# Optimization experiments

Hardware: AMD Instinct MI355X
Metric: run time of the kernel (lower is better)

## Reference

```python
import jax, jax.numpy as jnp
from jax import lax
import numpy as np

H_FEAT = 14
W_FEAT = 14
BN_EPS = 1e-5
NORM_EPS = 1e-12

def _coord_tensor():
    # Python-2 integer division as in the original repo
    c = np.zeros((H_FEAT * W_FEAT, 2), dtype=np.float32)
    for i in range(H_FEAT * W_FEAT):
        c[i, 0] = (i // W_FEAT - H_FEAT // 2) / (H_FEAT / 2.0)
        c[i, 1] = (i % W_FEAT - W_FEAT // 2) / (W_FEAT / 2.0)
    return jnp.asarray(c.reshape(1, H_FEAT, W_FEAT, 2).transpose(0, 3, 1, 2))  # [1,2,14,14]

def _l2norm(x, axis):
    n = jnp.linalg.norm(x, axis=axis, keepdims=True)
    return x / jnp.maximum(n, NORM_EPS)

def _conv2d(x, w, b, pad):
    y = lax.conv_general_dilated(x, w, (1, 1), [(pad, pad), (pad, pad)],
                                 dimension_numbers=("NCHW", "OIHW", "NCHW"))
    return y + b[None, :, None, None]

def _bn_train(x, g, b):
    m = x.mean(axis=(0, 2, 3), keepdims=True)
    v = x.var(axis=(0, 2, 3), keepdims=True)
    return (x - m) * lax.rsqrt(v + BN_EPS) * g[None, :, None, None] + b[None, :, None, None]

def _lstm_scan(emb, Wih, Whh, bih, bhh):
    # emb: [T, B, 300]; PyTorch gate order i,f,g,o
    Hdim = Whh.shape[1]
    B = emb.shape[1]
    def step(carry, x):
        h, c = carry
        gates = x @ Wih.T + h @ Whh.T + bih + bhh  # [B, 4H]
        i, f, g, o = jnp.split(gates, 4, axis=-1)
        c = jax.nn.sigmoid(f) * c + jax.nn.sigmoid(i) * jnp.tanh(g)
        h = jax.nn.sigmoid(o) * jnp.tanh(c)
        return (h, c), h
    init = (jnp.zeros((B, Hdim), emb.dtype), jnp.zeros((B, Hdim), emb.dtype))
    _, hs = lax.scan(step, init, emb)
    return hs  # [T, B, H]

def _resblock(v, coord, c1w, c1b, c2w, c2b, bng, bnb):
    B = v.shape[0]
    vin = jnp.concatenate([v, jnp.broadcast_to(coord, (B, 2, H_FEAT, W_FEAT))], axis=1)
    v1 = jax.nn.relu(_conv2d(vin, c1w, c1b, 0))
    v2 = jax.nn.relu(_bn_train(_conv2d(v1, c2w, c2b, 1), bng, bnb))
    return v2 + v1

def setup_inputs() -> dict:
    key = jax.random.key(0)
    ks = jax.random.split(key, 24)
    B, T, V, E = 128, 45, 10000, 300
    Hh = 1024
    s = 0.02
    inp = {}
    inp["que"] = jax.random.randint(ks[0], (B, T), 0, V, dtype=jnp.int64)
    inp["img"] = jax.random.normal(ks[1], (B, 1024, H_FEAT, W_FEAT), dtype=jnp.float32)
    inp["lookup"] = s * jax.random.normal(ks[2], (V + 1, E), dtype=jnp.float32)
    inp["Wih_f"] = s * jax.random.normal(ks[3], (4 * Hh, E), dtype=jnp.float32)
    inp["Whh_f"] = s * jax.random.normal(ks[4], (4 * Hh, Hh), dtype=jnp.float32)
    inp["bih_f"] = jnp.zeros((4 * Hh,), jnp.float32)
    inp["bhh_f"] = jnp.zeros((4 * Hh,), jnp.float32)
    inp["Wih_b"] = s * jax.random.normal(ks[5], (4 * Hh, E), dtype=jnp.float32)
    inp["Whh_b"] = s * jax.random.normal(ks[6], (4 * Hh, Hh), dtype=jnp.float32)
    inp["bih_b"] = jnp.zeros((4 * Hh,), jnp.float32)
    inp["bhh_b"] = jnp.zeros((4 * Hh,), jnp.float32)
    inp["conv0_w"] = s * jax.random.normal(ks[7], (128, 1026, 3, 3), dtype=jnp.float32)
    inp["conv0_b"] = jnp.zeros((128,), jnp.float32)
    inp["bn0_g"] = jnp.ones((128,), jnp.float32)
    inp["bn0_b"] = jnp.zeros((128,), jnp.float32)
    inp["r1c1_w"] = s * jax.random.normal(ks[8], (128, 130, 1, 1), dtype=jnp.float32)
    inp["r1c1_b"] = jnp.zeros((128,), jnp.float32)
    inp["r1c2_w"] = s * jax.random.normal(ks[9], (128, 128, 3, 3), dtype=jnp.float32)
    inp["r1c2_b"] = jnp.zeros((128,), jnp.float32)
    inp["r1bn_g"] = jnp.ones((128,), jnp.float32)
    inp["r1bn_b"] = jnp.zeros((128,), jnp.float32)
    inp["r2c1_w"] = s * jax.random.normal(ks[10], (128, 130, 1, 1), dtype=jnp.float32)
    inp["r2c1_b"] = jnp.zeros((128,), jnp.float32)
    inp["r2c2_w"] = s * jax.random.normal(ks[11], (128, 128, 3, 3), dtype=jnp.float32)
    inp["r2c2_b"] = jnp.zeros((128,), jnp.float32)
    inp["r2bn_g"] = jnp.ones((128,), jnp.float32)
    inp["r2bn_b"] = jnp.zeros((128,), jnp.float32)
    return inp

def reference(que, img, lookup, Wih_f, Whh_f, bih_f, bhh_f, Wih_b, Whh_b, bih_b, bhh_b,
              conv0_w, conv0_b, bn0_g, bn0_b,
              r1c1_w, r1c1_b, r1c2_w, r1c2_b, r1bn_g, r1bn_b,
              r2c1_w, r2c1_b, r2c2_w, r2c2_b, r2bn_g, r2bn_b):
    coord = _coord_tensor()
    # ---- encoder (LSTM mode) ----
    emb = lookup[que]                      # [B, T, 300]
    emb = jnp.transpose(emb, (1, 0, 2))    # [T, B, 300]
    h_f = _lstm_scan(emb, Wih_f, Whh_f, bih_f, bhh_f)
    h_b = _lstm_scan(emb[::-1], Wih_b, Whh_b, bih_b, bhh_b)[::-1]
    qenc = _l2norm(jnp.concatenate([h_f, h_b], axis=-1), axis=-1)  # [T, B, 2048]
    enc = qenc[-1]                                                  # [B, 2048]
    # ---- image branch ----
    v = _l2norm(img, axis=1)               # per-pixel L2 norm over 1024 channels
    B = v.shape[0]
    v = jnp.concatenate([v, jnp.broadcast_to(coord, (B, 2, H_FEAT, W_FEAT))], axis=1)
    v = jax.nn.relu(_bn_train(_conv2d(v, conv0_w, conv0_b, 1), bn0_g, bn0_b))
    v = _resblock(v, coord, r1c1_w, r1c1_b, r1c2_w, r1c2_b, r1bn_g, r1bn_b)
    v = _resblock(v, coord, r2c1_w, r2c1_b, r2c2_w, r2c2_b, r2bn_g, r2bn_b)
    return (enc, v)
```

## Files before the change

### kernel.cpp

```cpp
#include <hip/hip_runtime.h>
#include <math.h>

#define BB   128
#define T    45
#define E    300
#define HH   1024
#define G4   4096
#define HW   196
#define NPX  (BB*HW)
#define C0   1026
#define CM   128
#define CR   130
#define TCH  15

static __device__ __forceinline__ float sigm(float x) { return 1.f / (1.f + __expf(-x)); }

__global__ void k_embed(const int* __restrict__ que, const float* __restrict__ lookup,
                        float* __restrict__ emb) {
    int idx = blockIdx.x * 256 + threadIdx.x;
    if (idx >= T * BB * E) return;
    int e = idx % E;
    int n = idx / E;
    int b = n % BB;
    int t = n / BB;
    int q = que[b * T + t];
    emb[idx] = lookup[(size_t)q * E + e];
}

template <int BM, int BN, int TM, int TN>
__global__ __launch_bounds__(256) void k_gemm_nt(
    const float* __restrict__ A, int lda,
    const float* __restrict__ Bw, int ldb,
    const float* __restrict__ add,
    const float* __restrict__ bias,
    float* __restrict__ C, int ldc,
    int M, int N, int K, int relu) {
    constexpr int KT = 16;
    constexpr int TX = BN / TN;
    __shared__ alignas(16) float As[KT][BM + 4];
    __shared__ alignas(16) float Bs[KT][BN + 4];
    const int tid = threadIdx.x;
    const int tx = tid % TX, ty = tid / TX;
    const int r0 = blockIdx.x * BM, c0 = blockIdx.y * BN;
    float acc[TM][TN] = {};
    for (int k0 = 0; k0 < K; k0 += KT) {
#pragma unroll
        for (int l = tid; l < BM * KT; l += 256) {
            int m = l / KT, k = l % KT;
            int gm = r0 + m, gk = k0 + k;
            As[k][m] = (gm < M && gk < K) ? A[(size_t)gm * lda + gk] : 0.f;
        }
#pragma unroll
        for (int l = tid; l < BN * KT; l += 256) {
            int n = l / KT, k = l % KT;
            int gn = c0 + n, gk = k0 + k;
            Bs[k][n] = (gn < N && gk < K) ? Bw[(size_t)gn * ldb + gk] : 0.f;
        }
        __syncthreads();
#pragma unroll
        for (int k = 0; k < KT; ++k) {
            float ar[TM], br[TN];
            if constexpr ((TM & 3) == 0) {
#pragma unroll
                for (int i = 0; i < TM; i += 4) {
                    float4 v = *(const float4*)&As[k][ty * TM + i];
                    ar[i] = v.x; ar[i + 1] = v.y; ar[i + 2] = v.z; ar[i + 3] = v.w;
                }
            } else if constexpr ((TM & 1) == 0) {
#pragma unroll
                for (int i = 0; i < TM; i += 2) {
                    float2 v = *(const float2*)&As[k][ty * TM + i];
                    ar[i] = v.x; ar[i + 1] = v.y;
                }
            } else {
#pragma unroll
                for (int i = 0; i < TM; ++i) ar[i] = As[k][ty * TM + i];
            }
            if constexpr ((TN & 3) == 0) {
#pragma unroll
                for (int j = 0; j < TN; j += 4) {
                    float4 v = *(const float4*)&Bs[k][tx * TN + j];
                    br[j] = v.x; br[j + 1] = v.y; br[j + 2] = v.z; br[j + 3] = v.w;
                }
            } else if constexpr ((TN & 1) == 0) {
#pragma unroll
                for (int j = 0; j < TN; j += 2) {
                    float2 v = *(const float2*)&Bs[k][tx * TN + j];
                    br[j] = v.x; br[j + 1] = v.y;
                }
            } else {
#pragma unroll
                for (int j = 0; j < TN; ++j) br[j] = Bs[k][tx * TN + j];
            }
#pragma unroll
            for (int i = 0; i < TM; ++i)
#pragma unroll
                for (int j = 0; j < TN; ++j) acc[i][j] += ar[i] * br[j];
        }
        __syncthreads();
    }
#pragma unroll
    for (int i = 0; i < TM; ++i) {
        int gm = r0 + ty * TM + i;
        if (gm >= M) continue;
#pragma unroll
        for (int j = 0; j < TN; ++j) {
            int gn = c0 + tx * TN + j;
            if (gn >= N) continue;
            float v = acc[i][j];
            if (add) v += add[(size_t)gm * ldc + gn];
            if (bias) v += bias[gn];
            if (relu) v = fmaxf(v, 0.f);
            C[(size_t)gm * ldc + gn] = v;
        }
    }
}

__global__ void k_pack_wih(const float* __restrict__ Wih, float* __restrict__ o) {
    int idx = blockIdx.x * 256 + threadIdx.x;
    if (idx >= G4 * E) return;
    int k = idx % E;
    int n = idx / E;
    o[idx] = Wih[(size_t)((n & 3) * HH + (n >> 2)) * E + k];
}
__global__ void k_pack_whh(const float* __restrict__ Whh, float* __restrict__ o) {
    int idx = blockIdx.x * 256 + threadIdx.x;
    if (idx >= G4 * HH) return;
    int k = idx & 1023;
    int n = idx >> 10;
    o[idx] = Whh[(size_t)((n & 3) * HH + (n >> 2)) * HH + k];
}
__global__ void k_pack_b4i(const float* __restrict__ bih, const float* __restrict__ bhh,
                           float* __restrict__ out) {
    int n = blockIdx.x * 256 + threadIdx.x;
    if (n >= G4) return;
    int r = (n & 3) * HH + (n >> 2);
    out[n] = bih[r] + bhh[r];
}
__global__ void k_biasadd(const float* __restrict__ bih, const float* __restrict__ bhh,
                          float* __restrict__ out) {
    int idx = blockIdx.x * 256 + threadIdx.x;
    if (idx < G4) out[idx] = bih[idx] + bhh[idx];
}

__global__ void k_cell_plain(float* __restrict__ h, float* __restrict__ c,
                             const float* __restrict__ gx, int first) {
    int idx = blockIdx.x * 256 + threadIdx.x;
    int b = idx >> 10, j = idx & 1023;
    size_t base = (size_t)b * G4 + j;
    float gi = gx[base], gf = gx[base + HH], gg = gx[base + 2 * HH], go = gx[base + 3 * HH];
    float cp = first ? 0.f : c[idx];
    float cn = sigm(gf) * cp + sigm(gi) * tanhf(gg);
    c[idx] = cn;
    h[idx] = sigm(go) * tanhf(cn);
}

__global__ __launch_bounds__(256) void k_lstm_fused(
    const float* __restrict__ h_in, float* __restrict__ c_io,
    const float* __restrict__ gx,
    const float* __restrict__ Wpk,
    float* __restrict__ h_out, int first) {
    __shared__ alignas(16) float As[16][36];
    __shared__ alignas(16) float Bs[16][68];
    const int tid = threadIdx.x;
    const int tx = tid & 15, ty = tid >> 4;
    const int r0 = blockIdx.x * 32;
    const int c0 = blockIdx.y * 64;
    const int ka = tid & 15, ma = tid >> 4;
    float acc[2][4] = {};

    if (!first) {
        const float* hrow0 = h_in + (size_t)(r0 + ma) * HH + ka;
        const float* hrow1 = h_in + (size_t)(r0 + ma + 16) * HH + ka;
        const float* wp0 = Wpk + (size_t)(c0 + ma) * HH + ka;
        float a0A = hrow0[0], a1A = hrow1[0];
        float b0A = wp0[0], b1A = wp0[16 * HH], b2A = wp0[32 * HH], b3A = wp0[48 * HH];
        float a0B = hrow0[16], a1B = hrow1[16];
        float b0B = wp0[16], b1B = wp0[16 * HH + 16], b2B = wp0[32 * HH + 16],
              b3B = wp0[48 * HH + 16];
        for (int k0 = 0; k0 < HH; k0 += 16) {
            As[ka][ma] = a0A;
            As[ka][ma + 16] = a1A;
            Bs[ka][ma] = b0A;
            Bs[ka][ma + 16] = b1A;
            Bs[ka][ma + 32] = b2A;
            Bs[ka][ma + 48] = b3A;
            __syncthreads();
            a0A = a0B; a1A = a1B; b0A = b0B; b1A = b1B; b2A = b2B; b3A = b3B;
            if (k0 + 32 < HH) {
                int o = k0 + 32;
                a0B = hrow0[o];
                a1B = hrow1[o];
                b0B = wp0[o];
                b1B = wp0[16 * HH + o];
                b2B = wp0[32 * HH + o];
                b3B = wp0[48 * HH + o];
            }
#pragma unroll
            for (int k = 0; k < 16; ++k) {
                float2 a2 = *(const float2*)&As[k][ty * 2];
                float4 b4 = *(const float4*)&Bs[k][tx * 4];
                acc[0][0] += a2.x * b4.x;
                acc[0][1] += a2.x * b4.y;
                acc[0][2] += a2.x * b4.z;
                acc[0][3] += a2.x * b4.w;
                acc[1][0] += a2.y * b4.x;
                acc[1][1] += a2.y * b4.y;
                acc[1][2] += a2.y * b4.z;
                acc[1][3] += a2.y * b4.w;
            }
            __syncthreads();
        }
    }
    const int jj4 = c0 + tx * 4;
    const int u = jj4 >> 2;
#pragma unroll
    for (int i = 0; i < 2; ++i) {
        int b = r0 + ty * 2 + i;
        float4 g4 = *(const float4*)&gx[(size_t)b * G4 + jj4];
        float gi = acc[i][0] + g4.x;
        float gf = acc[i][1] + g4.y;
        float gg = acc[i][2] + g4.z;
        float go = acc[i][3] + g4.w;
        size_t ci = (size_t)b * HH + u;
        float cp = first ? 0.f : c_io[ci];
        float cn = sigm(gf) * cp + sigm(gi) * tanhf(gg);
        c_io[ci] = cn;
        h_out[ci] = sigm(go) * tanhf(cn);
    }
}

__global__ void k_enc(const float* __restrict__ hf, const float* __restrict__ hb,
                      float* __restrict__ out) {
    int b = blockIdx.x;
    int tid = threadIdx.x;
    float vals[8];
    float ss = 0.f;
#pragma unroll
    for (int i = 0; i < 8; ++i) {
        int j = i * 256 + tid;
        float v = (j < HH) ? hf[(size_t)b * HH + j] : hb[(size_t)b * HH + (j - HH)];
        vals[i] = v;
        ss += v * v;
    }
    __shared__ float red[256];
    red[tid] = ss;
    __syncthreads();
    for (int s = 128; s > 0; s >>= 1) {
        if (tid < s) red[tid] += red[tid + s];
        __syncthreads();
    }
    float scale = 1.f / fmaxf(sqrtf(red[0]), 1e-12f);
#pragma unroll
    for (int i = 0; i < 8; ++i) out[(size_t)b * 2048 + i * 256 + tid] = vals[i] * scale;
}

__global__ void k_pixssq(const float* __restrict__ img, float* __restrict__ ssq) {
    int b = blockIdx.x >> 4;
    int cc = (blockIdx.x & 15) * 64;
    int p = threadIdx.x;
    if (p >= HW) return;
    const float* base = img + ((size_t)b * 1024 + cc) * HW + p;
    float acc = 0.f;
#pragma unroll 4
    for (int c = 0; c < 64; ++c) {
        float v = base[(size_t)c * HW];
        acc += v * v;
    }
    atomicAdd(&ssq[b * HW + p], acc);
}

__global__ void k_invn(float* __restrict__ ssq) {
    int i = blockIdx.x * 256 + threadIdx.x;
    if (i >= NPX) return;
    ssq[i] = 1.f / fmaxf(sqrtf(ssq[i]), 1e-12f);
}

__global__ void k_packB0(const float* __restrict__ w, float* __restrict__ o) {
    int idx = blockIdx.x * 256 + threadIdx.x;
    if (idx >= 8 * 9 * 1040 * 16) return;
    int oi = idx & 15;
    int r = idx >> 4;
    int c = r % 1040;
    int gt = r / 1040;
    int tap = gt % 9, ocg = gt / 9;
    o[idx] = (c < C0) ? w[((size_t)(ocg * 16 + oi) * C0 + c) * 9 + tap] : 0.f;
}
__global__ void k_packBpm(const float* __restrict__ w, float* __restrict__ o) {
    int idx = blockIdx.x * 256 + threadIdx.x;
    if (idx >= 8 * 9 * 128 * 16) return;
    int oi = idx & 15;
    int r = idx >> 4;
    int c = r % 128;
    int gt = r / 128;
    int tap = gt % 9, ocg = gt / 9;
    o[idx] = w[((size_t)(ocg * 16 + oi) * 128 + c) * 9 + tap];
}

static __device__ __forceinline__ void conv_swz1568(int id, int& g, int& ocg, int& z) {
    int s2 = (id & 7) * 196 + (id >> 3);
    g = s2 >> 4;
    int cb = s2 & 15;
    ocg = cb >> 1;
    z = cb & 1;
}

__global__ __launch_bounds__(128) void k_conv0(const float* __restrict__ img,
                                               const float* __restrict__ invn,
                                               const float* __restrict__ wpk,
                                               const float* __restrict__ bias,
                                               float* __restrict__ outParts) {
    __shared__ float As[8][292];
    const int tid = threadIdx.x;
    int g, ocg, z;
    conv_swz1568(blockIdx.x, g, ocg, z);
    const int kbeg = z ? 528 : 0;
    const int kend = z ? 1032 : 528;
    float* out = outParts + (size_t)z * NPX * CM;
    const int P0 = g * 256;
    const int gp1 = P0 + tid;
    const int gp2 = gp1 + 128;
    const int p1 = gp1 % HW, p2 = gp2 % HW;
    const int y1 = p1 / 14, x1 = p1 % 14;
    const int y2 = p2 / 14, x2 = p2 % 14;

    const float* sptr[3];
    float sinv[3], scy[3], scx[3];
#pragma unroll
    for (int j = 0; j < 3; ++j) {
        int s = tid + j * 128;
        int gp = P0 - 16 + s;
        bool ok = (s < 288) && (gp >= 0) && (gp < NPX);
        int gpc = ok ? gp : 0;
        int pp = gpc % HW;
        int bi = gpc / HW;
        sptr[j] = img + ((size_t)bi * 1024) * HW + pp;
        sinv[j] = ok ? invn[gpc] : 0.f;
        scy[j] = ok ? (float)(pp / 14 - 7) * (1.f / 7.f) : 0.f;
        scx[j] = ok ? (float)(pp % 14 - 7) * (1.f / 7.f) : 0.f;
    }

    float acc0[16] = {};
    float acc1[16] = {};
    for (int k0 = kbeg; k0 < kend; k0 += 8) {
        __syncthreads();
        if (k0 != 1024) {
#pragma unroll
            for (int j = 0; j < 3; ++j) {
                int s = tid + j * 128;
                if (j < 2 || s < 292) {
                    const float* pb = sptr[j] + (size_t)k0 * HW;
                    float inv = sinv[j];
#pragma unroll
                    for (int k = 0; k < 8; ++k) As[k][s] = pb[(size_t)k * HW] * inv;
                }
            }
        } else {
#pragma unroll
            for (int j = 0; j < 3; ++j) {
                int s = tid + j * 128;
                if (j < 2 || s < 292) {
                    As[0][s] = scy[j];
                    As[1][s] = scx[j];
#pragma unroll
                    for (int k = 2; k < 8; ++k) As[k][s] = 0.f;
                }
            }
        }
        __syncthreads();
        for (int tap = 0; tap < 9; ++tap) {
            const int ky = tap / 3 - 1, kx = tap % 3 - 1;
            const int d = ky * 14 + kx;
            const int of1 = ((unsigned)(y1 + ky) < 14u && (unsigned)(x1 + kx) < 14u)
                                ? (tid + 16 + d) : 288;
            const int of2 = ((unsigned)(y2 + ky) < 14u && (unsigned)(x2 + kx) < 14u)
                                ? (tid + 144 + d) : 288;
            const float4* __restrict__ wq =
                (const float4*)wpk + ((size_t)(ocg * 9 + tap) * 1040 + k0) * 4;
#pragma unroll
            for (int k = 0; k < 8; ++k) {
                float a = As[k][of1];
                float b = As[k][of2];
                float4 w0 = wq[0], w1 = wq[1], w2 = wq[2], w3 = wq[3];
                wq += 4;
                acc0[0]  += a * w0.x;  acc1[0]  += b * w0.x;
                acc0[1]  += a * w0.y;  acc1[1]  += b * w0.y;
                acc0[2]  += a * w0.z;  acc1[2]  += b * w0.z;
                acc0[3]  += a * w0.w;  acc1[3]  += b * w0.w;
                acc0[4]  += a * w1.x;  acc1[4]  += b * w1.x;
                acc0[5]  += a * w1.y;  acc1[5]  += b * w1.y;
                acc0[6]  += a * w1.z;  acc1[6]  += b * w1.z;
                acc0[7]  += a * w1.w;  acc1[7]  += b * w1.w;
                acc0[8]  += a * w2.x;  acc1[8]  += b * w2.x;
                acc0[9]  += a * w2.y;  acc1[9]  += b * w2.y;
                acc0[10] += a * w2.z;  acc1[10] += b * w2.z;
                acc0[11] += a * w2.w;  acc1[11] += b * w2.w;
                acc0[12] += a * w3.x;  acc1[12] += b * w3.x;
                acc0[13] += a * w3.y;  acc1[13] += b * w3.y;
                acc0[14] += a * w3.z;  acc1[14] += b * w3.z;
                acc0[15] += a * w3.w;  acc1[15] += b * w3.w;
            }
        }
    }
    const float* bp = bias + ocg * 16;
    float* op1 = out + (size_t)gp1 * CM + ocg * 16;
    float* op2 = out + (size_t)gp2 * CM + ocg * 16;
#pragma unroll
    for (int qq = 0; qq < 4; ++qq) {
        float b0 = z ? 0.f : bp[qq * 4 + 0];
        float b1 = z ? 0.f : bp[qq * 4 + 1];
        float b2 = z ? 0.f : bp[qq * 4 + 2];
        float b3 = z ? 0.f : bp[qq * 4 + 3];
        float4 r0, r1;
        r0.x = acc0[qq * 4 + 0] + b0;  r1.x = acc1[qq * 4 + 0] + b0;
        r0.y = acc0[qq * 4 + 1] + b1;  r1.y = acc1[qq * 4 + 1] + b1;
        r0.z = acc0[qq * 4 + 2] + b2;  r1.z = acc1[qq * 4 + 2] + b2;
        r0.w = acc0[qq * 4 + 3] + b3;  r1.w = acc1[qq * 4 + 3] + b3;
        *(float4*)&op1[qq * 4] = r0;
        *(float4*)&op2[qq * 4] = r1;
    }
}

__global__ __launch_bounds__(128) void k_conv_pm(const float* __restrict__ vin,
                                                 const float* __restrict__ wpk,
                                                 const float* __restrict__ bias,
                                                 float* __restrict__ outParts) {
    __shared__ float As[8][292];
    const int tid = threadIdx.x;
    int g, ocg, z;
    conv_swz1568(blockIdx.x, g, ocg, z);
    const int kbeg = z * 64;
    float* out = outParts + (size_t)z * NPX * CM;
    const int P0 = g * 256;
    const int gp1 = P0 + tid;
    const int gp2 = gp1 + 128;
    const int p1 = gp1 % HW, p2 = gp2 % HW;
    const int y1 = p1 / 14, x1 = p1 % 14;
    const int y2 = p2 / 14, x2 = p2 % 14;

    const float* sptr[3];
    float smask[3];
#pragma unroll
    for (int j = 0; j < 3; ++j) {
        int s = tid + j * 128;
        int gp = P0 - 16 + s;
        bool ok = (s < 288) && (gp >= 0) && (gp < NPX);
        sptr[j] = vin + (size_t)(ok ? gp : 0) * CM;
        smask[j] = ok ? 1.f : 0.f;
    }

    float acc0[16] = {};
    float acc1[16] = {};
    for (int k0 = kbeg; k0 < kbeg + 64; k0 += 8) {
        __syncthreads();
#pragma unroll
        for (int j = 0; j < 3; ++j) {
            int s = tid + j * 128;
            if (j < 2 || s < 292) {
                float4 v0 = *(const float4*)&sptr[j][k0];
                float4 v1 = *(const float4*)&sptr[j][k0 + 4];
                float m = smask[j];
                As[0][s] = v0.x * m;
                As[1][s] = v0.y * m;
                As[2][s] = v0.z * m;
                As[3][s] = v0.w * m;
                As[4][s] = v1.x * m;
                As[5][s] = v1.y * m;
                As[6][s] = v1.z * m;
                As[7][s] = v1.w * m;
            }
        }
        __syncthreads();
        for (int tap = 0; tap < 9; ++tap) {
            const int ky = tap / 3 - 1, kx = tap % 3 - 1;
            const int d = ky * 14 + kx;
            const int of1 = ((unsigned)(y1 + ky) < 14u && (unsigned)(x1 + kx) < 14u)
                                ? (tid + 16 + d) : 288;
            const int of2 = ((unsigned)(y2 + ky) < 14u && (unsigned)(x2 + kx) < 14u)
                                ? (tid + 144 + d) : 288;
            const float4* __restrict__ wq =
                (const float4*)wpk + ((size_t)(ocg * 9 + tap) * 128 + k0) * 4;
#pragma unroll
            for (int k = 0; k < 8; ++k) {
                float a = As[k][of1];
                float b = As[k][of2];
                float4 w0 = wq[0], w1 = wq[1], w2 = wq[2], w3 = wq[3];
                wq += 4;
                acc0[0]  += a * w0.x;  acc1[0]  += b * w0.x;
                acc0[1]  += a * w0.y;  acc1[1]  += b * w0.y;
                acc0[2]  += a * w0.z;  acc1[2]  += b * w0.z;
                acc0[3]  += a * w0.w;  acc1[3]  += b * w0.w;
                acc0[4]  += a * w1.x;  acc1[4]  += b * w1.x;
                acc0[5]  += a * w1.y;  acc1[5]  += b * w1.y;
                acc0[6]  += a * w1.z;  acc1[6]  += b * w1.z;
                acc0[7]  += a * w1.w;  acc1[7]  += b * w1.w;
                acc0[8]  += a * w2.x;  acc1[8]  += b * w2.x;
                acc0[9]  += a * w2.y;  acc1[9]  += b * w2.y;
                acc0[10] += a * w2.z;  acc1[10] += b * w2.z;
                acc0[11] += a * w2.w;  acc1[11] += b * w2.w;
                acc0[12] += a * w3.x;  acc1[12] += b * w3.x;
                acc0[13] += a * w3.y;  acc1[13] += b * w3.y;
                acc0[14] += a * w3.z;  acc1[14] += b * w3.z;
                acc0[15] += a * w3.w;  acc1[15] += b * w3.w;
            }
        }
    }
    const float* bp = bias + ocg * 16;
    float* op1 = out + (size_t)gp1 * CM + ocg * 16;
    float* op2 = out + (size_t)gp2 * CM + ocg * 16;
#pragma unroll
    for (int qq = 0; qq < 4; ++qq) {
        float b0 = z ? 0.f : bp[qq * 4 + 0];
        float b1 = z ? 0.f : bp[qq * 4 + 1];
        float b2 = z ? 0.f : bp[qq * 4 + 2];
        float b3 = z ? 0.f : bp[qq * 4 + 3];
        float4 r0, r1;
        r0.x = acc0[qq * 4 + 0] + b0;  r1.x = acc1[qq * 4 + 0] + b0;
        r0.y = acc0[qq * 4 + 1] + b1;  r1.y = acc1[qq * 4 + 1] + b1;
        r0.z = acc0[qq * 4 + 2] + b2;  r1.z = acc1[qq * 4 + 2] + b2;
        r0.w = acc0[qq * 4 + 3] + b3;  r1.w = acc1[qq * 4 + 3] + b3;
        *(float4*)&op1[qq * 4] = r0;
        *(float4*)&op2[qq * 4] = r1;
    }
}

__global__ void k_bnstats(const float* __restrict__ xa, const float* __restrict__ xb,
                          float* __restrict__ stats) {
    int r0 = blockIdx.x * 224;
    int c = threadIdx.x & 127, rh = threadIdx.x >> 7;
    float s = 0.f, ss = 0.f;
    for (int r = r0 + rh; r < r0 + 224; r += 2) {
        float v = xa[(size_t)r * CM + c] + xb[(size_t)r * CM + c];
        s += v;
        ss += v * v;
    }
    __shared__ float rs[256], rss[256];
    rs[threadIdx.x] = s;
    rss[threadIdx.x] = ss;
    __syncthreads();
    if (threadIdx.x < 128) {
        s = rs[threadIdx.x] + rs[threadIdx.x + 128];
        ss = rss[threadIdx.x] + rss[threadIdx.x + 128];
        atomicAdd(&stats[c], s);
        atomicAdd(&stats[128 + c], ss);
    }
}

__global__ void k_bnfinal(const float* __restrict__ stats, const float* __restrict__ g,
                          const float* __restrict__ b, float* __restrict__ scsh) {
    int c = threadIdx.x;
    if (c >= 128) return;
    float mean = stats[c] / (float)NPX;
    float var = stats[128 + c] / (float)NPX - mean * mean;
    float sc = g[c] * rsqrtf(var + 1e-5f);
    scsh[c] = sc;
    scsh[128 + c] = b[c] - mean * sc;
}

__global__ void k_apply_cat(const float* __restrict__ xa, const float* __restrict__ xb,
                            const float* __restrict__ scsh,
                            const float* __restrict__ addv, float* __restrict__ vinr) {
    int idx = blockIdx.x * 256 + threadIdx.x;
    if (idx >= NPX * CM) return;
    int c = idx & 127;
    int p = idx >> 7;
    float v = fmaxf((xa[idx] + xb[idx]) * scsh[c] + scsh[128 + c], 0.f);
    if (addv) v += addv[idx];
    vinr[(size_t)p * CR + c] = v;
}

__global__ void k_coords_r(float* __restrict__ vinr) {
    int p = blockIdx.x * 256 + threadIdx.x;
    if (p >= NPX) return;
    int pp = p % HW;
    int y = pp / 14, x = pp % 14;
    vinr[(size_t)p * CR + 128] = (float)(y - 7) * (1.f / 7.f);
    vinr[(size_t)p * CR + 129] = (float)(x - 7) * (1.f / 7.f);
}

__global__ void k_final(const float* __restrict__ xa, const float* __restrict__ xb,
                        const float* __restrict__ scsh,
                        const float* __restrict__ addv, float* __restrict__ outv) {
    int idx = blockIdx.x * 256 + threadIdx.x;
    if (idx >= NPX * CM) return;
    int p = idx % HW;
    int o = (idx / HW) & 127;
    int b = idx / (HW * CM);
    size_t pm = ((size_t)b * HW + p) * CM + o;
    outv[idx] = fmaxf((xa[pm] + xb[pm]) * scsh[o] + scsh[128 + o], 0.f) + addv[pm];
}

extern "C" void kernel_launch(void* const* d_in, const int* in_sizes, int n_in,
                              void* d_out, int out_size, void* d_ws, size_t ws_size,
                              hipStream_t stream) {
    const int* que = (const int*)d_in[0];
    const float* img = (const float*)d_in[1];
    const float* lookup = (const float*)d_in[2];
    const float* Wih_f = (const float*)d_in[3];
    const float* Whh_f = (const float*)d_in[4];
    const float* bih_f = (const float*)d_in[5];
    const float* bhh_f = (const float*)d_in[6];
    const float* Wih_b = (const float*)d_in[7];
    const float* bih_b = (const float*)d_in[9];
    const float* bhh_b = (const float*)d_in[10];
    const float* conv0_w = (const float*)d_in[11];
    const float* conv0_b = (const float*)d_in[12];
    const float* bn0_g = (const float*)d_in[13];
    const float* bn0_b = (const float*)d_in[14];
    const float* r1c1_w = (const float*)d_in[15];
    const float* r1c1_b = (const float*)d_in[16];
    const float* r1c2_w = (const float*)d_in[17];
    const float* r1c2_b = (const float*)d_in[18];
    const float* r1bn_g = (const float*)d_in[19];
    const float* r1bn_b = (const float*)d_in[20];
    const float* r2c1_w = (const float*)d_in[21];
    const float* r2c1_b = (const float*)d_in[22];
    const float* r2c2_w = (const float*)d_in[23];
    const float* r2c2_b = (const float*)d_in[24];
    const float* r2bn_g = (const float*)d_in[25];
    const float* r2bn_b = (const float*)d_in[26];
    float* out = (float*)d_out;

    float* ws = (float*)d_ws;
    float* emb = ws;
    float* Xg = emb + 1728000;
    float* WihPk = Xg + 7864320;
    float* WhhPk = WihPk + 1228800;
    float* b4i = WhhPk + 4194304;
    float* b4b = b4i + 4096;
    float* Xb = b4b + 4096;
    float* hA = Xb + 524288;
    float* hB = hA + 131072;
    float* cbuf = hB + 131072;
    float* hbb = cbuf + 131072;
    size_t lstm_end = (size_t)(hbb + 131072 - ws);
    float* invn = ws;
    float* wpk0 = invn + 25088;
    float* wpk1 = wpk0 + 1198080;
    float* wpk2 = wpk1 + 147456;
    float* xa = wpk2 + 147456;
    float* xb = xa + 3211264;
    float* vinr = xb + 3211264;
    float* v1 = vinr + 3261440;
    float* stats = v1 + 3211264;
    float* scsh = stats + 256;
    size_t img_end = (size_t)(scsh + 256 - ws);
    size_t need = (lstm_end > img_end ? lstm_end : img_end) * 4;
    if (ws_size < need) return;

    auto cdiv = [](int a, int b) { return (a + b - 1) / b; };
    const size_t BG = (size_t)BB * G4;

    k_embed<<<cdiv(T * BB * E, 256), 256, 0, stream>>>(que, lookup, emb);
    k_pack_wih<<<cdiv(G4 * E, 256), 256, 0, stream>>>(Wih_f, WihPk);
    k_pack_whh<<<cdiv(G4 * HH, 256), 256, 0, stream>>>(Whh_f, WhhPk);
    k_pack_b4i<<<16, 256, 0, stream>>>(bih_f, bhh_f, b4i);
    k_biasadd<<<16, 256, 0, stream>>>(bih_b, bhh_b, b4b);
    k_gemm_nt<64, 64, 4, 4><<<dim3(2, 64), 256, 0, stream>>>(
        emb + (size_t)(T - 1) * BB * E, E, Wih_b, E, nullptr, b4b, Xb, G4, BB, G4, E, 0);
    k_cell_plain<<<512, 256, 0, stream>>>(hbb, cbuf, Xb, 1);
    float* hp = hA;
    float* hq = hB;
    float* hlast = hA;
    for (int ch = 0; ch < 3; ++ch) {
        int t0 = ch * TCH;
        k_gemm_nt<64, 128, 4, 8><<<dim3(30, 32), 256, 0, stream>>>(
            emb + (size_t)t0 * BB * E, E, WihPk, E, nullptr, b4i, Xg, G4,
            TCH * BB, G4, E, 0);
        for (int s = 0; s < TCH; ++s) {
            int t = t0 + s;
            k_lstm_fused<<<dim3(4, 64), 256, 0, stream>>>(
                hq, cbuf, Xg + (size_t)s * BG, WhhPk, hp, (t == 0) ? 1 : 0);
            hlast = hp;
            float* tmp = hp; hp = hq; hq = tmp;
        }
    }
    k_enc<<<128, 256, 0, stream>>>(hlast, hbb, out);

    hipMemsetAsync(invn, 0, NPX * 4, stream);
    k_pixssq<<<BB * 16, 256, 0, stream>>>(img, invn);
    k_invn<<<cdiv(NPX, 256), 256, 0, stream>>>(invn);
    k_packB0<<<cdiv(8 * 9 * 1040 * 16, 256), 256, 0, stream>>>(conv0_w, wpk0);
    k_packBpm<<<cdiv(8 * 9 * 128 * 16, 256), 256, 0, stream>>>(r1c2_w, wpk1);
    k_packBpm<<<cdiv(8 * 9 * 128 * 16, 256), 256, 0, stream>>>(r2c2_w, wpk2);

    k_conv0<<<1568, 128, 0, stream>>>(img, invn, wpk0, conv0_b, xa);
    hipMemsetAsync(stats, 0, 256 * 4, stream);
    k_bnstats<<<112, 256, 0, stream>>>(xa, xb, stats);
    k_bnfinal<<<1, 128, 0, stream>>>(stats, bn0_g, bn0_b, scsh);
    k_apply_cat<<<cdiv(NPX * CM, 256), 256, 0, stream>>>(xa, xb, scsh, nullptr, vinr);
    k_coords_r<<<cdiv(NPX, 256), 256, 0, stream>>>(vinr);

    k_gemm_nt<128, 64, 8, 4><<<dim3(196, 2), 256, 0, stream>>>(
        vinr, CR, r1c1_w, CR, nullptr, r1c1_b, v1, CM, NPX, CM, CR, 1);
    k_conv_pm<<<1568, 128, 0, stream>>>(v1, wpk1, r1c2_b, xa);
    hipMemsetAsync(stats, 0, 256 * 4, stream);
    k_bnstats<<<112, 256, 0, stream>>>(xa, xb, stats);
    k_bnfinal<<<1, 128, 0, stream>>>(stats, r1bn_g, r1bn_b, scsh);
    k_apply_cat<<<cdiv(NPX * CM, 256), 256, 0, stream>>>(xa, xb, scsh, v1, vinr);

    k_gemm_nt<128, 64, 8, 4><<<dim3(196, 2), 256, 0, stream>>>(
        vinr, CR, r2c1_w, CR, nullptr, r2c1_b, v1, CM, NPX, CM, CR, 1);
    k_conv_pm<<<1568, 128, 0, stream>>>(v1, wpk2, r2c2_b, xa);
    hipMemsetAsync(stats, 0, 256 * 4, stream);
    k_bnstats<<<112, 256, 0, stream>>>(xa, xb, stats);
    k_bnfinal<<<1, 128, 0, stream>>>(stats, r2bn_g, r2bn_b, scsh);
    k_final<<<cdiv(NPX * CM, 256), 256, 0, stream>>>(xa, xb, scsh, v1, out + (size_t)BB * 2048);
}
```

Before: 3.605 ms.

## Halve conv0 output-channel tile, fold BN finalize and coords into apply kernels

The first 3x3 conv now gives each block 8 output channels instead of 16. Its packed weights, swizzle and grid are changed to match, doubling the block count to 3136. This lowers per-thread accumulator registers and adds parallelism, at the cost of reloading and rescaling the 1026-channel input tile twice as often. Separately, the BN-finalize kernel and the coordinate-fill kernel are removed: scale and shift are recomputed per element inside the apply and final kernels, and the coords are written there too. That saves several small launches but adds redundant rsqrt work per element.

```diff
diff --git a/kernel.cpp b/kernel.cpp
--- a/kernel.cpp
+++ b/kernel.cpp
@@ -278,13 +278,13 @@
 
 __global__ void k_packB0(const float* __restrict__ w, float* __restrict__ o) {
     int idx = blockIdx.x * 256 + threadIdx.x;
-    if (idx >= 8 * 9 * 1040 * 16) return;
-    int oi = idx & 15;
-    int r = idx >> 4;
+    if (idx >= 16 * 9 * 1040 * 8) return;
+    int oi = idx & 7;
+    int r = idx >> 3;
     int c = r % 1040;
     int gt = r / 1040;
     int tap = gt % 9, ocg = gt / 9;
-    o[idx] = (c < C0) ? w[((size_t)(ocg * 16 + oi) * C0 + c) * 9 + tap] : 0.f;
+    o[idx] = (c < C0) ? w[((size_t)(ocg * 8 + oi) * C0 + c) * 9 + tap] : 0.f;
 }
 __global__ void k_packBpm(const float* __restrict__ w, float* __restrict__ o) {
     int idx = blockIdx.x * 256 + threadIdx.x;
@@ -297,6 +297,13 @@
     o[idx] = w[((size_t)(ocg * 16 + oi) * 128 + c) * 9 + tap];
 }
 
+static __device__ __forceinline__ void conv_swz3136(int id, int& g, int& ocg, int& z) {
+    int s2 = (id & 7) * 392 + (id >> 3);
+    g = s2 >> 5;
+    int cb = s2 & 31;
+    ocg = cb >> 1;
+    z = cb & 1;
+}
 static __device__ __forceinline__ void conv_swz1568(int id, int& g, int& ocg, int& z) {
     int s2 = (id & 7) * 196 + (id >> 3);
     g = s2 >> 4;
@@ -313,7 +320,7 @@
     __shared__ float As[8][292];
     const int tid = threadIdx.x;
     int g, ocg, z;
-    conv_swz1568(blockIdx.x, g, ocg, z);
+    conv_swz3136(blockIdx.x, g, ocg, z);
     const int kbeg = z ? 528 : 0;
     const int kend = z ? 1032 : 528;
     float* out = outParts + (size_t)z * NPX * CM;
@@ -340,8 +347,8 @@
         scx[j] = ok ? (float)(pp % 14 - 7) * (1.f / 7.f) : 0.f;
     }
 
-    float acc0[16] = {};
-    float acc1[16] = {};
+    float acc0[8] = {};
+    float acc1[8] = {};
     for (int k0 = kbeg; k0 < kend; k0 += 8) {
         __syncthreads();
         if (k0 != 1024) {
@@ -376,7 +383,102 @@
             const int of2 = ((unsigned)(y2 + ky) < 14u && (unsigned)(x2 + kx) < 14u)
                                 ? (tid + 144 + d) : 288;
             const float4* __restrict__ wq =
-                (const float4*)wpk + ((size_t)(ocg * 9 + tap) * 1040 + k0) * 4;
+                (const float4*)wpk + ((size_t)(ocg * 9 + tap) * 1040 + k0) * 2;
+#pragma unroll
+            for (int k = 0; k < 8; ++k) {
+                float a = As[k][of1];
+                float b = As[k][of2];
+                float4 w0 = wq[0], w1 = wq[1];
+                wq += 2;
+                acc0[0] += a * w0.x;  acc1[0] += b * w0.x;
+                acc0[1] += a * w0.y;  acc1[1] += b * w0.y;
+                acc0[2] += a * w0.z;  acc1[2] += b * w0.z;
+                acc0[3] += a * w0.w;  acc1[3] += b * w0.w;
+                acc0[4] += a * w1.x;  acc1[4] += b * w1.x;
+                acc0[5] += a * w1.y;  acc1[5] += b * w1.y;
+                acc0[6] += a * w1.z;  acc1[6] += b * w1.z;
+                acc0[7] += a * w1.w;  acc1[7] += b * w1.w;
+            }
+        }
+    }
+    const float* bp = bias + ocg * 8;
+    float* op1 = out + (size_t)gp1 * CM + ocg * 8;
+    float* op2 = out + (size_t)gp2 * CM + ocg * 8;
+#pragma unroll
+    for (int qq = 0; qq < 2; ++qq) {
+        float b0 = z ? 0.f : bp[qq * 4 + 0];
+        float b1 = z ? 0.f : bp[qq * 4 + 1];
+        float b2 = z ? 0.f : bp[qq * 4 + 2];
+        float b3 = z ? 0.f : bp[qq * 4 + 3];
+        float4 r0, r1;
+        r0.x = acc0[qq * 4 + 0] + b0;  r1.x = acc1[qq * 4 + 0] + b0;
+        r0.y = acc0[qq * 4 + 1] + b1;  r1.y = acc1[qq * 4 + 1] + b1;
+        r0.z = acc0[qq * 4 + 2] + b2;  r1.z = acc1[qq * 4 + 2] + b2;
+        r0.w = acc0[qq * 4 + 3] + b3;  r1.w = acc1[qq * 4 + 3] + b3;
+        *(float4*)&op1[qq * 4] = r0;
+        *(float4*)&op2[qq * 4] = r1;
+    }
+}
+
+__global__ __launch_bounds__(128) void k_conv_pm(const float* __restrict__ vin,
+                                                 const float* __restrict__ wpk,
+                                                 const float* __restrict__ bias,
+                                                 float* __restrict__ outParts) {
+    __shared__ float As[8][292];
+    const int tid = threadIdx.x;
+    int g, ocg, z;
+    conv_swz1568(blockIdx.x, g, ocg, z);
+    const int kbeg = z * 64;
+    float* out = outParts + (size_t)z * NPX * CM;
+    const int P0 = g * 256;
+    const int gp1 = P0 + tid;
+    const int gp2 = gp1 + 128;
+    const int p1 = gp1 % HW, p2 = gp2 % HW;
+    const int y1 = p1 / 14, x1 = p1 % 14;
+    const int y2 = p2 / 14, x2 = p2 % 14;
+
+    const float* sptr[3];
+    float smask[3];
+#pragma unroll
+    for (int j = 0; j < 3; ++j) {
+        int s = tid + j * 128;
+        int gp = P0 - 16 + s;
+        bool ok = (s < 288) && (gp >= 0) && (gp < NPX);
+        sptr[j] = vin + (size_t)(ok ? gp : 0) * CM;
+        smask[j] = ok ? 1.f : 0.f;
+    }
+
+    float acc0[16] = {};
+    float acc1[16] = {};
+    for (int k0 = kbeg; k0 < kbeg + 64; k0 += 8) {
+        __syncthreads();
+#pragma unroll
+        for (int j = 0; j < 3; ++j) {
+            int s = tid + j * 128;
+            if (j < 2 || s < 292) {
+                float4 v0 = *(const float4*)&sptr[j][k0];
+                float4 v1 = *(const float4*)&sptr[j][k0 + 4];
+                float m = smask[j];
+                As[0][s] = v0.x * m;
+                As[1][s] = v0.y * m;
+                As[2][s] = v0.z * m;
+                As[3][s] = v0.w * m;
+                As[4][s] = v1.x * m;
+                As[5][s] = v1.y * m;
+                As[6][s] = v1.z * m;
+                As[7][s] = v1.w * m;
+            }
+        }
+        __syncthreads();
+        for (int tap = 0; tap < 9; ++tap) {
+            const int ky = tap / 3 - 1, kx = tap % 3 - 1;
+            const int d = ky * 14 + kx;
+            const int of1 = ((unsigned)(y1 + ky) < 14u && (unsigned)(x1 + kx) < 14u)
+                                ? (tid + 16 + d) : 288;
+            const int of2 = ((unsigned)(y2 + ky) < 14u && (unsigned)(x2 + kx) < 14u)
+                                ? (tid + 144 + d) : 288;
+            const float4* __restrict__ wq =
+                (const float4*)wpk + ((size_t)(ocg * 9 + tap) * 128 + k0) * 4;
 #pragma unroll
             for (int k = 0; k < 8; ++k) {
                 float a = As[k][of1];
@@ -421,109 +523,6 @@
     }
 }
 
-__global__ __launch_bounds__(128) void k_conv_pm(const float* __restrict__ vin,
-                                                 const float* __restrict__ wpk,
-                                                 const float* __restrict__ bias,
-                                                 float* __restrict__ outParts) {
-    __shared__ float As[8][292];
-    const int tid = threadIdx.x;
-    int g, ocg, z;
-    conv_swz1568(blockIdx.x, g, ocg, z);
-    const int kbeg = z * 64;
-    float* out = outParts + (size_t)z * NPX * CM;
-    const int P0 = g * 256;
-    const int gp1 = P0 + tid;
-    const int gp2 = gp1 + 128;
-    const int p1 = gp1 % HW, p2 = gp2 % HW;
-    const int y1 = p1 / 14, x1 = p1 % 14;
-    const int y2 = p2 / 14, x2 = p2 % 14;
-
-    const float* sptr[3];
-    float smask[3];
-#pragma unroll
-    for (int j = 0; j < 3; ++j) {
-        int s = tid + j * 128;
-        int gp = P0 - 16 + s;
-        bool ok = (s < 288) && (gp >= 0) && (gp < NPX);
-        sptr[j] = vin + (size_t)(ok ? gp : 0) * CM;
-        smask[j] = ok ? 1.f : 0.f;
-    }
-
-    float acc0[16] = {};
-    float acc1[16] = {};
-    for (int k0 = kbeg; k0 < kbeg + 64; k0 += 8) {
-        __syncthreads();
-#pragma unroll
-        for (int j = 0; j < 3; ++j) {
-            int s = tid + j * 128;
-            if (j < 2 || s < 292) {
-                float4 v0 = *(const float4*)&sptr[j][k0];
-                float4 v1 = *(const float4*)&sptr[j][k0 + 4];
-                float m = smask[j];
-                As[0][s] = v0.x * m;
-                As[1][s] = v0.y * m;
-                As[2][s] = v0.z * m;
-                As[3][s] = v0.w * m;
-                As[4][s] = v1.x * m;
-                As[5][s] = v1.y * m;
-                As[6][s] = v1.z * m;
-                As[7][s] = v1.w * m;
-            }
-        }
-        __syncthreads();
-        for (int tap = 0; tap < 9; ++tap) {
-            const int ky = tap / 3 - 1, kx = tap % 3 - 1;
-            const int d = ky * 14 + kx;
-            const int of1 = ((unsigned)(y1 + ky) < 14u && (unsigned)(x1 + kx) < 14u)
-                                ? (tid + 16 + d) : 288;
-            const int of2 = ((unsigned)(y2 + ky) < 14u && (unsigned)(x2 + kx) < 14u)
-                                ? (tid + 144 + d) : 288;
-            const float4* __restrict__ wq =
-                (const float4*)wpk + ((size_t)(ocg * 9 + tap) * 128 + k0) * 4;
-#pragma unroll
-            for (int k = 0; k < 8; ++k) {
-                float a = As[k][of1];
-                float b = As[k][of2];
-                float4 w0 = wq[0], w1 = wq[1], w2 = wq[2], w3 = wq[3];
-                wq += 4;
-                acc0[0]  += a * w0.x;  acc1[0]  += b * w0.x;
-                acc0[1]  += a * w0.y;  acc1[1]  += b * w0.y;
-                acc0[2]  += a * w0.z;  acc1[2]  += b * w0.z;
-                acc0[3]  += a * w0.w;  acc1[3]  += b * w0.w;
-                acc0[4]  += a * w1.x;  acc1[4]  += b * w1.x;
-                acc0[5]  += a * w1.y;  acc1[5]  += b * w1.y;
-                acc0[6]  += a * w1.z;  acc1[6]  += b * w1.z;
-                acc0[7]  += a * w1.w;  acc1[7]  += b * w1.w;
-                acc0[8]  += a * w2.x;  acc1[8]  += b * w2.x;
-                acc0[9]  += a * w2.y;  acc1[9]  += b * w2.y;
-                acc0[10] += a * w2.z;  acc1[10] += b * w2.z;
-                acc0[11] += a * w2.w;  acc1[11] += b * w2.w;
-                acc0[12] += a * w3.x;  acc1[12] += b * w3.x;
-                acc0[13] += a * w3.y;  acc1[13] += b * w3.y;
-                acc0[14] += a * w3.z;  acc1[14] += b * w3.z;
-                acc0[15] += a * w3.w;  acc1[15] += b * w3.w;
-            }
-        }
-    }
-    const float* bp = bias + ocg * 16;
-    float* op1 = out + (size_t)gp1 * CM + ocg * 16;
-    float* op2 = out + (size_t)gp2 * CM + ocg * 16;
-#pragma unroll
-    for (int qq = 0; qq < 4; ++qq) {
-        float b0 = z ? 0.f : bp[qq * 4 + 0];
-        float b1 = z ? 0.f : bp[qq * 4 + 1];
-        float b2 = z ? 0.f : bp[qq * 4 + 2];
-        float b3 = z ? 0.f : bp[qq * 4 + 3];
-        float4 r0, r1;
-        r0.x = acc0[qq * 4 + 0] + b0;  r1.x = acc1[qq * 4 + 0] + b0;
-        r0.y = acc0[qq * 4 + 1] + b1;  r1.y = acc1[qq * 4 + 1] + b1;
-        r0.z = acc0[qq * 4 + 2] + b2;  r1.z = acc1[qq * 4 + 2] + b2;
-        r0.w = acc0[qq * 4 + 3] + b3;  r1.w = acc1[qq * 4 + 3] + b3;
-        *(float4*)&op1[qq * 4] = r0;
-        *(float4*)&op2[qq * 4] = r1;
-    }
-}
-
 __global__ void k_bnstats(const float* __restrict__ xa, const float* __restrict__ xb,
                           float* __restrict__ stats) {
     int r0 = blockIdx.x * 224;
@@ -546,48 +545,44 @@
     }
 }
 
-__global__ void k_bnfinal(const float* __restrict__ stats, const float* __restrict__ g,
-                          const float* __restrict__ b, float* __restrict__ scsh) {
-    int c = threadIdx.x;
-    if (c >= 128) return;
-    float mean = stats[c] / (float)NPX;
-    float var = stats[128 + c] / (float)NPX - mean * mean;
-    float sc = g[c] * rsqrtf(var + 1e-5f);
-    scsh[c] = sc;
-    scsh[128 + c] = b[c] - mean * sc;
-}
-
 __global__ void k_apply_cat(const float* __restrict__ xa, const float* __restrict__ xb,
-                            const float* __restrict__ scsh,
+                            const float* __restrict__ stats,
+                            const float* __restrict__ gg, const float* __restrict__ bb,
                             const float* __restrict__ addv, float* __restrict__ vinr) {
     int idx = blockIdx.x * 256 + threadIdx.x;
     if (idx >= NPX * CM) return;
     int c = idx & 127;
     int p = idx >> 7;
-    float v = fmaxf((xa[idx] + xb[idx]) * scsh[c] + scsh[128 + c], 0.f);
+    float mean = stats[c] * (1.f / (float)NPX);
+    float var = stats[128 + c] * (1.f / (float)NPX) - mean * mean;
+    float sc = gg[c] * rsqrtf(var + 1e-5f);
+    float sh = bb[c] - mean * sc;
+    float v = fmaxf((xa[idx] + xb[idx]) * sc + sh, 0.f);
     if (addv) v += addv[idx];
     vinr[(size_t)p * CR + c] = v;
-}
-
-__global__ void k_coords_r(float* __restrict__ vinr) {
-    int p = blockIdx.x * 256 + threadIdx.x;
-    if (p >= NPX) return;
-    int pp = p % HW;
-    int y = pp / 14, x = pp % 14;
-    vinr[(size_t)p * CR + 128] = (float)(y - 7) * (1.f / 7.f);
-    vinr[(size_t)p * CR + 129] = (float)(x - 7) * (1.f / 7.f);
+    if (c < 2) {
+        int pp = p % HW;
+        float cv = (c == 0) ? (float)(pp / 14 - 7) * (1.f / 7.f)
+                            : (float)(pp % 14 - 7) * (1.f / 7.f);
+        vinr[(size_t)p * CR + 128 + c] = cv;
+    }
 }
 
 __global__ void k_final(const float* __restrict__ xa, const float* __restrict__ xb,
-                        const float* __restrict__ scsh,
+                        const float* __restrict__ stats,
+                        const float* __restrict__ gg, const float* __restrict__ bb,
                         const float* __restrict__ addv, float* __restrict__ outv) {
     int idx = blockIdx.x * 256 + threadIdx.x;
     if (idx >= NPX * CM) return;
     int p = idx % HW;
     int o = (idx / HW) & 127;
     int b = idx / (HW * CM);
+    float mean = stats[o] * (1.f / (float)NPX);
+    float var = stats[128 + o] * (1.f / (float)NPX) - mean * mean;
+    float sc = gg[o] * rsqrtf(var + 1e-5f);
+    float sh = bb[o] - mean * sc;
     size_t pm = ((size_t)b * HW + p) * CM + o;
-    outv[idx] = fmaxf((xa[pm] + xb[pm]) * scsh[o] + scsh[128 + o], 0.f) + addv[pm];
+    outv[idx] = fmaxf((xa[pm] + xb[pm]) * sc + sh, 0.f) + addv[pm];
 }
 
 extern "C" void kernel_launch(void* const* d_in, const int* in_sizes, int n_in,
@@ -643,8 +638,7 @@
     float* vinr = xb + 3211264;
     float* v1 = vinr + 3261440;
     float* stats = v1 + 3211264;
-    float* scsh = stats + 256;
-    size_t img_end = (size_t)(scsh + 256 - ws);
+    size_t img_end = (size_t)(stats + 256 - ws);
     size_t need = (lstm_end > img_end ? lstm_end : img_end) * 4;
     if (ws_size < need) return;
 
@@ -680,30 +674,29 @@
     hipMemsetAsync(invn, 0, NPX * 4, stream);
     k_pixssq<<<BB * 16, 256, 0, stream>>>(img, invn);
     k_invn<<<cdiv(NPX, 256), 256, 0, stream>>>(invn);
-    k_packB0<<<cdiv(8 * 9 * 1040 * 16, 256), 256, 0, stream>>>(conv0_w, wpk0);
+    k_packB0<<<cdiv(16 * 9 * 1040 * 8, 256), 256, 0, stream>>>(conv0_w, wpk0);
     k_packBpm<<<cdiv(8 * 9 * 128 * 16, 256), 256, 0, stream>>>(r1c2_w, wpk1);
     k_packBpm<<<cdiv(8 * 9 * 128 * 16, 256), 256, 0, stream>>>(r2c2_w, wpk2);
 
-    k_conv0<<<1568, 128, 0, stream>>>(img, invn, wpk0, conv0_b, xa);
+    k_conv0<<<3136, 128, 0, stream>>>(img, invn, wpk0, conv0_b, xa);
     hipMemsetAsync(stats, 0, 256 * 4, stream);
     k_bnstats<<<112, 256, 0, stream>>>(xa, xb, stats);
-    k_bnfinal<<<1, 128, 0, stream>>>(stats, bn0_g, bn0_b, scsh);
-    k_apply_cat<<<cdiv(NPX * CM, 256), 256, 0, stream>>>(xa, xb, scsh, nullptr, vinr);
-    k_coords_r<<<cdiv(NPX, 256), 256, 0, stream>>>(vinr);
+    k_apply_cat<<<cdiv(NPX * CM, 256), 256, 0, stream>>>(xa, xb, stats, bn0_g, bn0_b,
+                                                         nullptr, vinr);
 
     k_gemm_nt<128, 64, 8, 4><<<dim3(196, 2), 256, 0, stream>>>(
         vinr, CR, r1c1_w, CR, nullptr, r1c1_b, v1, CM, NPX, CM, CR, 1);
     k_conv_pm<<<1568, 128, 0, stream>>>(v1, wpk1, r1c2_b, xa);
     hipMemsetAsync(stats, 0, 256 * 4, stream);
     k_bnstats<<<112, 256, 0, stream>>>(xa, xb, stats);
-    k_bnfinal<<<1, 128, 0, stream>>>(stats, r1bn_g, r1bn_b, scsh);
-    k_apply_cat<<<cdiv(NPX * CM, 256), 256, 0, stream>>>(xa, xb, scsh, v1, vinr);
+    k_apply_cat<<<cdiv(NPX * CM, 256), 256, 0, stream>>>(xa, xb, stats, r1bn_g, r1bn_b,
+                                                         v1, vinr);
 
     k_gemm_nt<128, 64, 8, 4><<<dim3(196, 2), 256, 0, stream>>>(
         vinr, CR, r2c1_w, CR, nullptr, r2c1_b, v1, CM, NPX, CM, CR, 1);
     k_conv_pm<<<1568, 128, 0, stream>>>(v1, wpk2, r2c2_b, xa);
     hipMemsetAsync(stats, 0, 256 * 4, stream);
     k_bnstats<<<112, 256, 0, stream>>>(xa, xb, stats);
-    k_bnfinal<<<1, 128, 0, stream>>>(stats, r2bn_g, r2bn_b, scsh);
-    k_final<<<cdiv(NPX * CM, 256), 256, 0, stream>>>(xa, xb, scsh, v1, out + (size_t)BB * 2048);
-}
+    k_final<<<cdiv(NPX * CM, 256), 256, 0, stream>>>(xa, xb, stats, r2bn_g, r2bn_b,
+                                                     v1, out + (size_t)BB * 2048);
+}
```

New measurement: 3.607 ms. Within noise of the previous version (+0.1%).
